# Optimization experiments

Hardware: AMD Instinct MI355X
Metric: run time of the kernel (lower is better)

The kernel has to match this reference:

```python
import jax, jax.numpy as jnp
import numpy as np

B, S, E, H, NE, K = 4, 1024, 1024, 16, 8, 2
DFF = 4 * E
DH = E // H
EPS = 1e-5


def _ln(x, g, b):
    m = jnp.mean(x, axis=-1, keepdims=True)
    v = jnp.mean(jnp.square(x - m), axis=-1, keepdims=True)
    return (x - m) * jax.lax.rsqrt(v + EPS) * g + b


def setup_inputs() -> dict:
    key = jax.random.key(0)
    ks = jax.random.split(key, 20)
    n = lambda k, sh, s: (jax.random.normal(k, sh, jnp.float32) * s)
    return {
        'x': n(ks[0], (B, S, E), 1.0),
        'ln1_g': jnp.ones((E,), jnp.float32), 'ln1_b': jnp.zeros((E,), jnp.float32),
        'wq': n(ks[1], (E, E), 0.02), 'bq': jnp.zeros((E,), jnp.float32),
        'wk': n(ks[2], (E, E), 0.02), 'bk': jnp.zeros((E,), jnp.float32),
        'wv': n(ks[3], (E, E), 0.02), 'bv': jnp.zeros((E,), jnp.float32),
        'wo': n(ks[4], (E, E), 0.02), 'bo': jnp.zeros((E,), jnp.float32),
        'ln2_g': jnp.ones((E,), jnp.float32), 'ln2_b': jnp.zeros((E,), jnp.float32),
        'sw1': n(ks[5], (E, DFF), 0.02), 'sb1': jnp.zeros((DFF,), jnp.float32),
        'sw2': n(ks[6], (DFF, E), 0.02), 'sb2': jnp.zeros((E,), jnp.float32),
        'ew1': n(ks[7], (NE, E, DFF), 0.02), 'eb1': jnp.zeros((NE, DFF), jnp.float32),
        'ew2': n(ks[8], (NE, DFF, E), 0.02), 'eb2': jnp.zeros((NE, E), jnp.float32),
        'w_gate': n(ks[9], (E, NE), 1.0),
    }


def reference(x, ln1_g, ln1_b, wq, bq, wk, bk, wv, bv, wo, bo,
              ln2_g, ln2_b, sw1, sb1, sw2, sb2, ew1, eb1, ew2, eb2, w_gate):
    # --- self-attention sublayer (eval: no dropout) ---
    res1 = x
    h = _ln(x, ln1_g, ln1_b)
    q = (h @ wq + bq).reshape(B, S, H, DH)
    k = (h @ wk + bk).reshape(B, S, H, DH)
    v = (h @ wv + bv).reshape(B, S, H, DH)
    scores = jnp.einsum('bqhd,bkhd->bhqk', q, k) / jnp.sqrt(jnp.float32(DH))
    attn = jax.nn.softmax(scores, axis=-1)
    ctx = jnp.einsum('bhqk,bkhd->bqhd', attn, v).reshape(B, S, E)
    x = res1 + (ctx @ wo + bo)

    # --- MoE sublayer ---
    res2 = x
    h2 = _ln(x, ln2_g, ln2_b)
    shared = jax.nn.gelu(h2 @ sw1 + sb1, approximate=False) @ sw2 + sb2

    # router (eval: clean logits, no noise)
    logits = h2 @ w_gate                                  # (B,S,NE)
    top_vals, top_idx = jax.lax.top_k(logits, K)          # (B,S,K)
    top_gates = jax.nn.softmax(top_vals, axis=-1)
    onehot = jax.nn.one_hot(top_idx, NE, dtype=x.dtype)   # (B,S,K,NE)
    gates = jnp.einsum('bsk,bske->bse', top_gates, onehot)
    probs = jax.nn.softmax(logits, axis=-1).reshape(-1, NE)
    P = probs.mean(0)
    f = (gates > 0).astype(x.dtype).reshape(-1, NE).mean(0)
    aux_loss = NE * jnp.sum(P * f)

    # dense all-expert compute, gated combine (matches original math)
    eh = jax.nn.gelu(jnp.einsum('bse,neh->bnsh', h2, ew1) + eb1[None, :, None, :],
                     approximate=False)
    eo = jnp.einsum('bnsh,nhe->bnse', eh, ew2) + eb2[None, :, None, :]
    expert_out = jnp.einsum('bnse,bsn->bse', eo, gates)

    return res2 + shared + expert_out, aux_loss
```

## Files before the change

### kernel.cpp

```cpp
#include <hip/hip_runtime.h>
#include <stdint.h>

#define B_    4
#define S_    1024
#define E_    1024
#define H_    16
#define NE_   8
#define DFF_  4096
#define NT_   4096
#define QS_   3072
#define ROWCAP9_ 13440

typedef unsigned short u16;
typedef short bf16x8 __attribute__((ext_vector_type(8)));
typedef float f32x4 __attribute__((ext_vector_type(4)));

__device__ __forceinline__ float bf2f(u16 u){ unsigned v = ((unsigned)u) << 16; return __builtin_bit_cast(float, v); }
__device__ __forceinline__ u16 f2bf(float f){ unsigned x = __builtin_bit_cast(unsigned, f); return (u16)((x + 0x7FFFu + ((x >> 16) & 1u)) >> 16); }
__device__ __forceinline__ float gelu_f(float x){ return 0.5f * x * (1.f + erff(x * 0.70710678118f)); }

__device__ __forceinline__ void gl_lds16(const u16* g, u16* l){
  __builtin_amdgcn_global_load_lds((__attribute__((address_space(1))) void*)(const_cast<u16*>(g)),
                                   (__attribute__((address_space(3))) void*)(l), 16, 0, 0);
}

#define KSW32(l)   ((((l) & 3) ^ (((l) >> 3) & 3)) << 3)
#define FRAGOFF(l) (((l) & 15) * 32 + (((((l) >> 4) ^ (((l) >> 1) & 3))) << 3))

__launch_bounds__(256)
__global__ void ln_kernel(const float* __restrict__ x, const float* __restrict__ g,
                          const float* __restrict__ be, u16* __restrict__ out)
{
  const int row = blockIdx.x;
  const float4 v = ((const float4*)(x + (size_t)row * E_))[threadIdx.x];
  float s = v.x + v.y + v.z + v.w;
  #pragma unroll
  for(int mm = 32; mm >= 1; mm >>= 1) s += __shfl_xor(s, mm);
  __shared__ float red[8];
  const int wid = threadIdx.x >> 6;
  if((threadIdx.x & 63) == 0) red[wid] = s;
  __syncthreads();
  const float mean = (red[0] + red[1] + red[2] + red[3]) * (1.0f / E_);
  const float d0 = v.x - mean, d1 = v.y - mean, d2 = v.z - mean, d3 = v.w - mean;
  float q2 = d0*d0 + d1*d1 + d2*d2 + d3*d3;
  #pragma unroll
  for(int mm = 32; mm >= 1; mm >>= 1) q2 += __shfl_xor(q2, mm);
  if((threadIdx.x & 63) == 0) red[4 + wid] = q2;
  __syncthreads();
  const float var = (red[4] + red[5] + red[6] + red[7]) * (1.0f / E_);
  const float rs = rsqrtf(var + 1e-5f);
  const float4 gg = ((const float4*)g)[threadIdx.x];
  const float4 bb = ((const float4*)be)[threadIdx.x];
  ushort4 o;
  o.x = f2bf(d0 * rs * gg.x + bb.x);
  o.y = f2bf(d1 * rs * gg.y + bb.y);
  o.z = f2bf(d2 * rs * gg.z + bb.z);
  o.w = f2bf(d3 * rs * gg.w + bb.w);
  ((ushort4*)(out + (size_t)row * E_))[threadIdx.x] = o;
}

__launch_bounds__(256)
__global__ void ln_router_kernel(const float* __restrict__ x, const float* __restrict__ g,
                                 const float* __restrict__ be, u16* __restrict__ out,
                                 const float* __restrict__ wg,
                                 float* __restrict__ probs, float* __restrict__ tkgate,
                                 int* __restrict__ tkidx, int* __restrict__ counts)
{
  const int row = blockIdx.x;
  const int tid = threadIdx.x, lane = tid & 63, wid = tid >> 6;
  const float4 v = ((const float4*)(x + (size_t)row * E_))[tid];
  float s = v.x + v.y + v.z + v.w;
  #pragma unroll
  for(int mm = 32; mm >= 1; mm >>= 1) s += __shfl_xor(s, mm);
  __shared__ float red[8];
  __shared__ float part[4][8];
  if(lane == 0) red[wid] = s;
  __syncthreads();
  const float mean = (red[0] + red[1] + red[2] + red[3]) * (1.0f / E_);
  const float d0 = v.x - mean, d1 = v.y - mean, d2 = v.z - mean, d3 = v.w - mean;
  float q2 = d0*d0 + d1*d1 + d2*d2 + d3*d3;
  #pragma unroll
  for(int mm = 32; mm >= 1; mm >>= 1) q2 += __shfl_xor(q2, mm);
  if(lane == 0) red[4 + wid] = q2;
  __syncthreads();
  const float var = (red[4] + red[5] + red[6] + red[7]) * (1.0f / E_);
  const float rs = rsqrtf(var + 1e-5f);
  const float4 gg = ((const float4*)g)[tid];
  const float4 bb = ((const float4*)be)[tid];
  ushort4 o;
  o.x = f2bf(d0 * rs * gg.x + bb.x);
  o.y = f2bf(d1 * rs * gg.y + bb.y);
  o.z = f2bf(d2 * rs * gg.z + bb.z);
  o.w = f2bf(d3 * rs * gg.w + bb.w);
  ((ushort4*)(out + (size_t)row * E_))[tid] = o;
  const float h0 = bf2f(o.x), h1 = bf2f(o.y), h2v = bf2f(o.z), h3 = bf2f(o.w);
  float a[8];
  #pragma unroll
  for(int e = 0; e < 8; e++) a[e] = 0.f;
  const float* wr = wg + (size_t)(tid * 4) * NE_;
  #pragma unroll
  for(int j = 0; j < 4; j++){
    const float hj = (j == 0) ? h0 : (j == 1) ? h1 : (j == 2) ? h2v : h3;
    const float4 w0 = *(const float4*)(wr + j * NE_);
    const float4 w1 = *(const float4*)(wr + j * NE_ + 4);
    a[0] += hj * w0.x; a[1] += hj * w0.y; a[2] += hj * w0.z; a[3] += hj * w0.w;
    a[4] += hj * w1.x; a[5] += hj * w1.y; a[6] += hj * w1.z; a[7] += hj * w1.w;
  }
  #pragma unroll
  for(int mm = 1; mm < 64; mm <<= 1)
    #pragma unroll
    for(int e = 0; e < 8; e++) a[e] += __shfl_xor(a[e], mm);
  if(lane == 0)
    #pragma unroll
    for(int e = 0; e < 8; e++) part[wid][e] = a[e];
  __syncthreads();
  if(tid == 0){
    float lg[8];
    #pragma unroll
    for(int e = 0; e < 8; e++) lg[e] = part[0][e] + part[1][e] + part[2][e] + part[3][e];
    float mx = lg[0];
    #pragma unroll
    for(int e = 1; e < 8; e++) mx = fmaxf(mx, lg[e]);
    float se = 0.f, ex[8];
    #pragma unroll
    for(int e = 0; e < 8; e++){ ex[e] = expf(lg[e] - mx); se += ex[e]; }
    const float inv = 1.f / se;
    float* pr = probs + (size_t)row * 8;
    #pragma unroll
    for(int e = 0; e < 8; e++) pr[e] = ex[e] * inv;
    int i1 = 0; float v1 = lg[0];
    #pragma unroll
    for(int e = 1; e < 8; e++) if(lg[e] > v1){ v1 = lg[e]; i1 = e; }
    int i2 = -1; float v2 = -3.4e38f;
    #pragma unroll
    for(int e = 0; e < 8; e++) if(e != i1 && lg[e] > v2){ v2 = lg[e]; i2 = e; }
    const float t = expf(v2 - v1);
    tkidx[row*2] = i1; tkidx[row*2+1] = i2;
    tkgate[row*2] = 1.f / (1.f + t); tkgate[row*2+1] = t / (1.f + t);
    atomicAdd(&counts[i1], 1); atomicAdd(&counts[i2], 1);
  }
}

__device__ __forceinline__ void transpose_body(const float* __restrict__ W, u16* __restrict__ WT, int K, int N)
{
  __shared__ __align__(16) u16 t[64][72];
  const int k0 = blockIdx.x * 64, n0 = blockIdx.y * 64;
  const int tid = threadIdx.x;
  const int kr = tid >> 2;
  const int nc = (tid & 3) * 4;
  #pragma unroll
  for(int p = 0; p < 4; p++){
    float4 v = *(const float4*)(W + (size_t)(k0 + kr) * N + n0 + nc + p * 16);
    t[nc + p*16 + 0][kr] = f2bf(v.x);
    t[nc + p*16 + 1][kr] = f2bf(v.y);
    t[nc + p*16 + 2][kr] = f2bf(v.z);
    t[nc + p*16 + 3][kr] = f2bf(v.w);
  }
  __syncthreads();
  const int nr = tid >> 3;
  const int kg = (tid & 7) * 8;
  #pragma unroll
  for(int p = 0; p < 2; p++){
    const int nn = nr + p * 32;
    unsigned u0 = t[nn][kg+0], u1 = t[nn][kg+1], u2 = t[nn][kg+2], u3 = t[nn][kg+3];
    unsigned u4 = t[nn][kg+4], u5 = t[nn][kg+5], u6 = t[nn][kg+6], u7 = t[nn][kg+7];
    uint4 o;
    o.x = u0 | (u1 << 16); o.y = u2 | (u3 << 16); o.z = u4 | (u5 << 16); o.w = u6 | (u7 << 16);
    *(uint4*)(WT + (size_t)(n0 + nn) * K + k0 + kg) = o;
  }
}

__launch_bounds__(256)
__global__ void transpose_kernel(const float* __restrict__ W, u16* __restrict__ WT, int K, int N)
{ transpose_body(W, WT, K, N); }

__launch_bounds__(256)
__global__ void transpose4_kernel(const float* wq, const float* wk, const float* wv, const float* wo,
                                  u16* __restrict__ WT)
{
  const float* W = (blockIdx.z == 0) ? wq : (blockIdx.z == 1) ? wk : (blockIdx.z == 2) ? wv : wo;
  transpose_body(W, WT + (size_t)blockIdx.z * E_ * E_, E_, E_);
}

__launch_bounds__(256)
__global__ void transpose9_kernel(const float* __restrict__ ew, const float* __restrict__ sw,
                                  u16* __restrict__ WT, int K, int N)
{
  const float* W = (blockIdx.z < 8) ? (ew + (size_t)blockIdx.z * K * N) : sw;
  transpose_body(W, WT + (size_t)blockIdx.z * K * N, K, N);
}

__global__ void prep_kernel(const float* __restrict__ bq, const float* __restrict__ bk,
                            const float* __restrict__ bv, float* __restrict__ bcat,
                            int* __restrict__ counts, int* __restrict__ rowlist,
                            const float* __restrict__ eb1, const float* __restrict__ sb1,
                            float* __restrict__ b9up,
                            const float* __restrict__ eb2, const float* __restrict__ sb2,
                            float* __restrict__ b9dn)
{
  const int stride = gridDim.x * 256;
  for(int i = blockIdx.x * 256 + threadIdx.x; i < 9 * DFF_; i += stride){
    b9up[i] = (i < 8 * DFF_) ? eb1[i] : sb1[i - 8 * DFF_];
    if(i < 9 * E_)   b9dn[i] = (i < 8 * E_) ? eb2[i] : sb2[i - 8 * E_];
    if(i < QS_)      bcat[i] = (i < E_) ? bq[i] : (i < 2*E_) ? bk[i - E_] : bv[i - 2*E_];
    if(i < 16)       counts[i] = 0;
    if(i < ROWCAP9_) rowlist[i] = -1;
  }
}

template<int MODE>
__launch_bounds__(256)
__global__ void gemm_kernel(const u16* __restrict__ A, const u16* __restrict__ Bt,
                            int N, int Kd, const float* __restrict__ bias,
                            u16* __restrict__ outB)
{
  __shared__ __align__(16) u16 As0[4096], Bs0[4096], As1[4096], Bs1[4096];
  const int tid = threadIdx.x, lane = tid & 63, wid = tid >> 6;
  const int wm = wid >> 1, wn = wid & 1;
  const int tm = blockIdx.y * 128, tn = blockIdx.x * 128;

  const f32x4 zero = {0.f, 0.f, 0.f, 0.f};
  f32x4 acc[4][4];
  #pragma unroll
  for(int m = 0; m < 4; m++)
    #pragma unroll
    for(int n = 0; n < 4; n++) acc[m][n] = zero;

  const int ksw = KSW32(lane);
  const u16* gA0 = A  + (size_t)(tm + wid*32 + (lane >> 2)) * Kd + ksw;
  const u16* gA1 = gA0 + (size_t)16 * Kd;
  const u16* gB0 = Bt + (size_t)(tn + wid*32 + (lane >> 2)) * Kd + ksw;
  const u16* gB1 = gB0 + (size_t)16 * Kd;
  u16* lA0 = As0 + wid*1024; u16* lA1 = lA0 + 512;
  u16* lB0 = Bs0 + wid*1024; u16* lB1 = lB0 + 512;
  u16* lA0b = As1 + wid*1024; u16* lA1b = lA0b + 512;
  u16* lB0b = Bs1 + wid*1024; u16* lB1b = lB0b + 512;
  const int fo = FRAGOFF(lane);
  const int fA = wm * 2048, fB = wn * 2048;

  for(int k0 = 0; k0 < Kd; k0 += 64){
    __syncthreads();
    gl_lds16(gA0 + k0, lA0);  gl_lds16(gA1 + k0, lA1);
    gl_lds16(gB0 + k0, lB0);  gl_lds16(gB1 + k0, lB1);
    gl_lds16(gA0 + k0+32, lA0b); gl_lds16(gA1 + k0+32, lA1b);
    gl_lds16(gB0 + k0+32, lB0b); gl_lds16(gB1 + k0+32, lB1b);
    __syncthreads();
    bf16x8 aF[4], bF[4];
    #pragma unroll
    for(int m = 0; m < 4; m++) aF[m] = *(const bf16x8*)(As0 + fA + m*512 + fo);
    #pragma unroll
    for(int n = 0; n < 4; n++) bF[n] = *(const bf16x8*)(Bs0 + fB + n*512 + fo);
    #pragma unroll
    for(int m = 0; m < 4; m++)
      #pragma unroll
      for(int n = 0; n < 4; n++)
        acc[m][n] = __builtin_amdgcn_mfma_f32_16x16x32_bf16(aF[m], bF[n], acc[m][n], 0, 0, 0);
    #pragma unroll
    for(int m = 0; m < 4; m++) aF[m] = *(const bf16x8*)(As1 + fA + m*512 + fo);
    #pragma unroll
    for(int n = 0; n < 4; n++) bF[n] = *(const bf16x8*)(Bs1 + fB + n*512 + fo);
    #pragma unroll
    for(int m = 0; m < 4; m++)
      #pragma unroll
      for(int n = 0; n < 4; n++)
        acc[m][n] = __builtin_amdgcn_mfma_f32_16x16x32_bf16(aF[m], bF[n], acc[m][n], 0, 0, 0);
  }

  #pragma unroll
  for(int m = 0; m < 4; m++){
    const int row = tm + wm*64 + m*16 + ((lane >> 4) << 2);
    #pragma unroll
    for(int n = 0; n < 4; n++){
      const int col = tn + wn*64 + n*16 + (lane & 15);
      const float bc = bias[col];
      #pragma unroll
      for(int r = 0; r < 4; r++){
        const float v = acc[m][n][r] + bc;
        const size_t idx = (size_t)(row + r) * N + col;
        if constexpr(MODE == 0) outB[idx] = f2bf(v);
        else outB[idx] = f2bf(gelu_f(v));
      }
    }
  }
}

template<int MODE>
__launch_bounds__(256)
__global__ void gemm64_kernel(const u16* __restrict__ A, const u16* __restrict__ Bt,
                              int N, int Kd, const float* __restrict__ bias,
                              float* __restrict__ outF, const float* __restrict__ resid)
{
  __shared__ __align__(16) u16 As0[2048], As1[2048], Bs0[4096], Bs1[4096];
  const int tid = threadIdx.x, lane = tid & 63, wid = tid >> 6;
  const int wm = wid >> 1, wn = wid & 1;
  const int tm = blockIdx.y * 64, tn = blockIdx.x * 128;

  const f32x4 zero = {0.f, 0.f, 0.f, 0.f};
  f32x4 acc[2][4];
  #pragma unroll
  for(int m = 0; m < 2; m++)
    #pragma unroll
    for(int n = 0; n < 4; n++) acc[m][n] = zero;

  const int ksw = KSW32(lane);
  const u16* gA = A + (size_t)(tm + wid*16 + (lane >> 2)) * Kd + ksw;
  const u16* gB0 = Bt + (size_t)(tn + wid*32 + (lane >> 2)) * Kd + ksw;
  const u16* gB1 = gB0 + (size_t)16 * Kd;
  u16* lA  = As0 + wid*512;  u16* lAb = As1 + wid*512;
  u16* lB0 = Bs0 + wid*1024; u16* lB1 = lB0 + 512;
  u16* lB0b = Bs1 + wid*1024; u16* lB1b = lB0b + 512;
  const int fo = FRAGOFF(lane);
  const int fA = wm * 1024, fB = wn * 2048;

  for(int k0 = 0; k0 < Kd; k0 += 64){
    __syncthreads();
    gl_lds16(gA + k0, lA);
    gl_lds16(gB0 + k0, lB0); gl_lds16(gB1 + k0, lB1);
    gl_lds16(gA + k0+32, lAb);
    gl_lds16(gB0 + k0+32, lB0b); gl_lds16(gB1 + k0+32, lB1b);
    __syncthreads();
    bf16x8 aF[2], bF[4];
    #pragma unroll
    for(int m = 0; m < 2; m++) aF[m] = *(const bf16x8*)(As0 + fA + m*512 + fo);
    #pragma unroll
    for(int n = 0; n < 4; n++) bF[n] = *(const bf16x8*)(Bs0 + fB + n*512 + fo);
    #pragma unroll
    for(int m = 0; m < 2; m++)
      #pragma unroll
      for(int n = 0; n < 4; n++)
        acc[m][n] = __builtin_amdgcn_mfma_f32_16x16x32_bf16(aF[m], bF[n], acc[m][n], 0, 0, 0);
    #pragma unroll
    for(int m = 0; m < 2; m++) aF[m] = *(const bf16x8*)(As1 + fA + m*512 + fo);
    #pragma unroll
    for(int n = 0; n < 4; n++) bF[n] = *(const bf16x8*)(Bs1 + fB + n*512 + fo);
    #pragma unroll
    for(int m = 0; m < 2; m++)
      #pragma unroll
      for(int n = 0; n < 4; n++)
        acc[m][n] = __builtin_amdgcn_mfma_f32_16x16x32_bf16(aF[m], bF[n], acc[m][n], 0, 0, 0);
  }

  #pragma unroll
  for(int m = 0; m < 2; m++){
    const int row = tm + wm*32 + m*16 + ((lane >> 4) << 2);
    #pragma unroll
    for(int n = 0; n < 4; n++){
      const int col = tn + wn*64 + n*16 + (lane & 15);
      const float bc = bias[col];
      #pragma unroll
      for(int r = 0; r < 4; r++){
        const float v = acc[m][n][r] + bc;
        const size_t idx = (size_t)(row + r) * N + col;
        if constexpr(MODE == 2) outF[idx] = resid[idx] + v;
        else outF[idx] += v;
      }
    }
  }
}

__launch_bounds__(256)
__global__ void attn_kernel(const u16* __restrict__ qkv, u16* __restrict__ ctx)
{
  __shared__ __align__(16) u16 Ks[64 * 64];
  __shared__ __align__(16) u16 Vt[64 * 72];
  __shared__ __align__(16) u16 Ps[64 * 72];
  const int tid = threadIdx.x, lane = tid & 63, wid = tid >> 6;
  const int bh = blockIdx.y, bb = bh >> 4, hh = bh & 15;
  const int q0 = blockIdx.x * 64;
  const size_t tok0 = (size_t)bb * S_;
  const int hcol = hh * 64;

  bf16x8 aQ0, aQ1;
  {
    const u16* qp = qkv + (tok0 + q0 + wid*16 + (lane & 15)) * QS_ + hcol + ((lane >> 4) << 3);
    aQ0 = *(const bf16x8*)qp;
    aQ1 = *(const bf16x8*)(qp + 32);
  }
  const f32x4 zero = {0.f, 0.f, 0.f, 0.f};
  f32x4 accO[4]; float mrow[4], lrow[4];
  #pragma unroll
  for(int n = 0; n < 4; n++) accO[n] = zero;
  #pragma unroll
  for(int r = 0; r < 4; r++){ mrow[r] = -1e30f; lrow[r] = 0.f; }
  const float sc = 0.125f * 1.44269504f;
  const int ksw8 = (((lane & 7) ^ ((lane >> 3) & 7)) << 3);

  for(int kv0 = 0; kv0 < S_; kv0 += 64){
    __syncthreads();
    {
      const u16* gp = qkv + (tok0 + kv0 + wid*16 + (lane >> 3)) * QS_ + 1024 + hcol + ksw8;
      gl_lds16(gp, Ks + (wid*16) * 64);
      gl_lds16(gp + (size_t)8 * QS_, Ks + (wid*16 + 8) * 64);
    }
    {
      #pragma unroll
      for(int i = 0; i < 2; i++){
        const int tok = (tid >> 3) + i * 32;
        const int d0 = (tid & 7) << 3;
        bf16x8 vv = *(const bf16x8*)(qkv + (tok0 + kv0 + tok) * QS_ + 2048 + hcol + d0);
        #pragma unroll
        for(int j = 0; j < 8; j++) Vt[(d0 + j) * 72 + tok] = (u16)vv[j];
      }
    }
    __syncthreads();
    f32x4 sf[4];
    #pragma unroll
    for(int n = 0; n < 4; n++){
      const int rb = n*16 + (lane & 15);
      bf16x8 b0 = *(const bf16x8*)(Ks + rb*64 + ((((lane >> 4)    ) ^ (lane & 7)) << 3));
      bf16x8 b1 = *(const bf16x8*)(Ks + rb*64 + ((((lane >> 4) + 4) ^ (lane & 7)) << 3));
      f32x4 t = zero;
      t = __builtin_amdgcn_mfma_f32_16x16x32_bf16(aQ0, b0, t, 0, 0, 0);
      t = __builtin_amdgcn_mfma_f32_16x16x32_bf16(aQ1, b1, t, 0, 0, 0);
      sf[n] = t;
    }
    #pragma unroll
    for(int r = 0; r < 4; r++){
      const float s0 = sf[0][r]*sc, s1 = sf[1][r]*sc, s2 = sf[2][r]*sc, s3 = sf[3][r]*sc;
      float mx = fmaxf(fmaxf(s0, s1), fmaxf(s2, s3));
      #pragma unroll
      for(int mm = 1; mm < 16; mm <<= 1) mx = fmaxf(mx, __shfl_xor(mx, mm));
      const float mnew = fmaxf(mrow[r], mx);
      const float resc = exp2f(mrow[r] - mnew);
      mrow[r] = mnew;
      const float p0 = exp2f(s0 - mnew), p1 = exp2f(s1 - mnew);
      const float p2 = exp2f(s2 - mnew), p3 = exp2f(s3 - mnew);
      float ps = p0 + p1 + p2 + p3;
      #pragma unroll
      for(int mm = 1; mm < 16; mm <<= 1) ps += __shfl_xor(ps, mm);
      lrow[r] = lrow[r] * resc + ps;
      #pragma unroll
      for(int n = 0; n < 4; n++) accO[n][r] *= resc;
      const int prow = wid*16 + ((lane >> 4) << 2) + r;
      Ps[prow*72 +      (lane & 15)] = f2bf(p0);
      Ps[prow*72 + 16 + (lane & 15)] = f2bf(p1);
      Ps[prow*72 + 32 + (lane & 15)] = f2bf(p2);
      Ps[prow*72 + 48 + (lane & 15)] = f2bf(p3);
    }
    bf16x8 pa0 = *(const bf16x8*)(Ps + (wid*16 + (lane & 15)) * 72 + ((lane >> 4) << 3));
    bf16x8 pa1 = *(const bf16x8*)(Ps + (wid*16 + (lane & 15)) * 72 + 32 + ((lane >> 4) << 3));
    #pragma unroll
    for(int n = 0; n < 4; n++){
      bf16x8 b0 = *(const bf16x8*)(Vt + (n*16 + (lane & 15)) * 72 + ((lane >> 4) << 3));
      bf16x8 b1 = *(const bf16x8*)(Vt + (n*16 + (lane & 15)) * 72 + 32 + ((lane >> 4) << 3));
      accO[n] = __builtin_amdgcn_mfma_f32_16x16x32_bf16(pa0, b0, accO[n], 0, 0, 0);
      accO[n] = __builtin_amdgcn_mfma_f32_16x16x32_bf16(pa1, b1, accO[n], 0, 0, 0);
    }
  }
  const size_t cbase = tok0 * E_ + hcol;
  #pragma unroll
  for(int n = 0; n < 4; n++)
    #pragma unroll
    for(int r = 0; r < 4; r++){
      const int row = q0 + wid*16 + ((lane >> 4) << 2) + r;
      const int col = n*16 + (lane & 15);
      ctx[cbase + (size_t)row * E_ + col] = f2bf(accO[n][r] / lrow[r]);
    }
}

__global__ void scan_kernel(const int* __restrict__ counts, int* __restrict__ aoff,
                            int* __restrict__ cursor, int addShared)
{
  if(threadIdx.x == 0){
    int o = 0;
    for(int e = 0; e < 8; e++){
      aoff[e] = o; cursor[e] = o;
      o += ((counts[e] + 127) >> 7) << 7;
    }
    aoff[8] = o;
    aoff[9] = o + (addShared ? NT_ : 0);
  }
}

__global__ void build_kernel(const int* __restrict__ tkidx, const float* __restrict__ tkgate,
                             int* __restrict__ cursor, int* __restrict__ rowlist,
                             float* __restrict__ rowgate, const int* __restrict__ aoff, int addShared)
{
  const int t = blockIdx.x * 256 + threadIdx.x;
  if(t >= NT_) return;
  #pragma unroll
  for(int kk = 0; kk < 2; kk++){
    const int e = tkidx[t*2 + kk];
    const int pos = atomicAdd(&cursor[e], 1);
    rowlist[pos] = t; rowgate[pos] = tkgate[t*2 + kk];
  }
  if(addShared){
    const int base = aoff[8];
    rowlist[base + t] = t; rowgate[base + t] = 1.f;
  }
}

__launch_bounds__(256)
__global__ void upmoe_kernel(const u16* __restrict__ Ah2, const u16* __restrict__ W1T,
                             const float* __restrict__ b9up,
                             const int* __restrict__ rowlist, const int* __restrict__ aoff,
                             u16* __restrict__ ehid)
{
  const int rowTile = blockIdx.y * 128;
  if(rowTile >= aoff[9]) return;
  int e = 0;
  #pragma unroll
  for(int i = 1; i <= 8; i++) if(rowTile >= aoff[i]) e = i;
  __shared__ __align__(16) u16 As0[4096], Bs0[4096], As1[4096], Bs1[4096];
  const int tid = threadIdx.x, lane = tid & 63, wid = tid >> 6;
  const int wm = wid >> 1, wn = wid & 1;
  const int tn = blockIdx.x * 128;
  const u16* Bt = W1T + (size_t)e * DFF_ * E_;

  const int r0 = rowTile + wid*32 + (lane >> 2);
  int t0 = rowlist[r0];      if(t0 < 0) t0 = 0;
  int t1 = rowlist[r0 + 16]; if(t1 < 0) t1 = 0;
  const int ksw = KSW32(lane);
  const u16* gA0 = Ah2 + (size_t)t0 * E_ + ksw;
  const u16* gA1 = Ah2 + (size_t)t1 * E_ + ksw;
  const u16* gB0 = Bt + (size_t)(tn + wid*32 + (lane >> 2)) * E_ + ksw;
  const u16* gB1 = gB0 + (size_t)16 * E_;
  u16* lA0 = As0 + wid*1024; u16* lA1 = lA0 + 512;
  u16* lB0 = Bs0 + wid*1024; u16* lB1 = lB0 + 512;
  u16* lA0b = As1 + wid*1024; u16* lA1b = lA0b + 512;
  u16* lB0b = Bs1 + wid*1024; u16* lB1b = lB0b + 512;
  const int fo = FRAGOFF(lane);
  const int fA = wm * 2048, fB = wn * 2048;

  const f32x4 zero = {0.f,0.f,0.f,0.f};
  f32x4 acc[4][4];
  #pragma unroll
  for(int m = 0; m < 4; m++)
    #pragma unroll
    for(int n = 0; n < 4; n++) acc[m][n] = zero;

  for(int k0 = 0; k0 < E_; k0 += 64){
    __syncthreads();
    gl_lds16(gA0 + k0, lA0);  gl_lds16(gA1 + k0, lA1);
    gl_lds16(gB0 + k0, lB0);  gl_lds16(gB1 + k0, lB1);
    gl_lds16(gA0 + k0+32, lA0b); gl_lds16(gA1 + k0+32, lA1b);
    gl_lds16(gB0 + k0+32, lB0b); gl_lds16(gB1 + k0+32, lB1b);
    __syncthreads();
    bf16x8 aF[4], bF[4];
    #pragma unroll
    for(int m = 0; m < 4; m++) aF[m] = *(const bf16x8*)(As0 + fA + m*512 + fo);
    #pragma unroll
    for(int n = 0; n < 4; n++) bF[n] = *(const bf16x8*)(Bs0 + fB + n*512 + fo);
    #pragma unroll
    for(int m = 0; m < 4; m++)
      #pragma unroll
      for(int n = 0; n < 4; n++)
        acc[m][n] = __builtin_amdgcn_mfma_f32_16x16x32_bf16(aF[m], bF[n], acc[m][n], 0, 0, 0);
    #pragma unroll
    for(int m = 0; m < 4; m++) aF[m] = *(const bf16x8*)(As1 + fA + m*512 + fo);
    #pragma unroll
    for(int n = 0; n < 4; n++) bF[n] = *(const bf16x8*)(Bs1 + fB + n*512 + fo);
    #pragma unroll
    for(int m = 0; m < 4; m++)
      #pragma unroll
      for(int n = 0; n < 4; n++)
        acc[m][n] = __builtin_amdgcn_mfma_f32_16x16x32_bf16(aF[m], bF[n], acc[m][n], 0, 0, 0);
  }
  #pragma unroll
  for(int m = 0; m < 4; m++){
    const int row = rowTile + wm*64 + m*16 + ((lane >> 4) << 2);
    #pragma unroll
    for(int n = 0; n < 4; n++){
      const int col = tn + wn*64 + n*16 + (lane & 15);
      const float bc = b9up[e * DFF_ + col];
      #pragma unroll
      for(int r = 0; r < 4; r++)
        ehid[(size_t)(row + r) * DFF_ + col] = f2bf(gelu_f(acc[m][n][r] + bc));
    }
  }
}

__launch_bounds__(256)
__global__ void downmoe_kernel(const u16* __restrict__ ehid, const u16* __restrict__ W2T,
                               const float* __restrict__ b9dn,
                               const int* __restrict__ rowlist, const float* __restrict__ rowgate,
                               const int* __restrict__ aoff, float* __restrict__ outF)
{
  const int nwg = (int)(gridDim.x * gridDim.y);
  const int b_lin = (int)(blockIdx.x + blockIdx.y * gridDim.x);
  const int b2 = (b_lin & 7) * (nwg >> 3) + (b_lin >> 3);
  const int bx = b2 & 7, by = b2 >> 3;
  const int rowTile = by * 64;
  if(rowTile >= aoff[9]) return;
  int e = 0;
  #pragma unroll
  for(int i = 1; i <= 8; i++) if(rowTile >= aoff[i]) e = i;
  __shared__ __align__(16) u16 As0[2048], As1[2048], Bs0[4096], Bs1[4096];
  const int tid = threadIdx.x, lane = tid & 63, wid = tid >> 6;
  const int wm = wid >> 1, wn = wid & 1;
  const int tn = bx * 128;
  const u16* Bt = W2T + (size_t)e * E_ * DFF_;

  const int ksw = KSW32(lane);
  const u16* gA = ehid + (size_t)(rowTile + wid*16 + (lane >> 2)) * DFF_ + ksw;
  const u16* gB0 = Bt + (size_t)(tn + wid*32 + (lane >> 2)) * DFF_ + ksw;
  const u16* gB1 = gB0 + (size_t)16 * DFF_;
  u16* lA  = As0 + wid*512;  u16* lAb = As1 + wid*512;
  u16* lB0 = Bs0 + wid*1024; u16* lB1 = lB0 + 512;
  u16* lB0b = Bs1 + wid*1024; u16* lB1b = lB0b + 512;
  const int fo = FRAGOFF(lane);
  const int fA = wm * 1024, fB = wn * 2048;

  const f32x4 zero = {0.f,0.f,0.f,0.f};
  f32x4 acc[2][4];
  #pragma unroll
  for(int m = 0; m < 2; m++)
    #pragma unroll
    for(int n = 0; n < 4; n++) acc[m][n] = zero;

  for(int k0 = 0; k0 < DFF_; k0 += 64){
    __syncthreads();
    gl_lds16(gA + k0, lA);
    gl_lds16(gB0 + k0, lB0); gl_lds16(gB1 + k0, lB1);
    gl_lds16(gA + k0+32, lAb);
    gl_lds16(gB0 + k0+32, lB0b); gl_lds16(gB1 + k0+32, lB1b);
    __syncthreads();
    bf16x8 aF[2], bF[4];
    #pragma unroll
    for(int m = 0; m < 2; m++) aF[m] = *(const bf16x8*)(As0 + fA + m*512 + fo);
    #pragma unroll
    for(int n = 0; n < 4; n++) bF[n] = *(const bf16x8*)(Bs0 + fB + n*512 + fo);
    #pragma unroll
    for(int m = 0; m < 2; m++)
      #pragma unroll
      for(int n = 0; n < 4; n++)
        acc[m][n] = __builtin_amdgcn_mfma_f32_16x16x32_bf16(aF[m], bF[n], acc[m][n], 0, 0, 0);
    #pragma unroll
    for(int m = 0; m < 2; m++) aF[m] = *(const bf16x8*)(As1 + fA + m*512 + fo);
    #pragma unroll
    for(int n = 0; n < 4; n++) bF[n] = *(const bf16x8*)(Bs1 + fB + n*512 + fo);
    #pragma unroll
    for(int m = 0; m < 2; m++)
      #pragma unroll
      for(int n = 0; n < 4; n++)
        acc[m][n] = __builtin_amdgcn_mfma_f32_16x16x32_bf16(aF[m], bF[n], acc[m][n], 0, 0, 0);
  }
  #pragma unroll
  for(int m = 0; m < 2; m++){
    const int row = rowTile + wm*32 + m*16 + ((lane >> 4) << 2);
    #pragma unroll
    for(int r = 0; r < 4; r++){
      const int rr = row + r;
      const int tok = rowlist[rr];
      if(tok < 0) continue;
      const float g = rowgate[rr];
      #pragma unroll
      for(int n = 0; n < 4; n++){
        const int col = tn + wn*64 + n*16 + (lane & 15);
        atomicAdd(&outF[(size_t)tok * E_ + col], g * (acc[m][n][r] + b9dn[e * E_ + col]));
      }
    }
  }
}

__launch_bounds__(256)
__global__ void aux_kernel(const float* __restrict__ probs, const int* __restrict__ counts,
                           float* __restrict__ outaux)
{
  float a[8];
  #pragma unroll
  for(int e = 0; e < 8; e++) a[e] = 0.f;
  for(int t = threadIdx.x; t < NT_; t += 256){
    const float* p = probs + (size_t)t * 8;
    #pragma unroll
    for(int e = 0; e < 8; e++) a[e] += p[e];
  }
  #pragma unroll
  for(int mm = 1; mm < 64; mm <<= 1)
    #pragma unroll
    for(int e = 0; e < 8; e++) a[e] += __shfl_xor(a[e], mm);
  __shared__ float part[4][8];
  const int wid = threadIdx.x >> 6;
  if((threadIdx.x & 63) == 0)
    for(int e = 0; e < 8; e++) part[wid][e] = a[e];
  __syncthreads();
  if(threadIdx.x == 0){
    float aux = 0.f;
    for(int e = 0; e < 8; e++){
      const float P = (part[0][e] + part[1][e] + part[2][e] + part[3][e]) / (float)NT_;
      const float f = (float)counts[e] / (float)NT_;
      aux += P * f;
    }
    outaux[0] = (float)NE_ * aux;
  }
}

extern "C" void kernel_launch(void* const* d_in, const int* in_sizes, int n_in,
                              void* d_out, int out_size, void* d_ws, size_t ws_size,
                              hipStream_t stream)
{
  (void)in_sizes; (void)n_in; (void)out_size;
  const float* x    = (const float*)d_in[0];
  const float* ln1g = (const float*)d_in[1];
  const float* ln1b = (const float*)d_in[2];
  const float* wq   = (const float*)d_in[3];
  const float* bq   = (const float*)d_in[4];
  const float* wk   = (const float*)d_in[5];
  const float* bk   = (const float*)d_in[6];
  const float* wv   = (const float*)d_in[7];
  const float* bv   = (const float*)d_in[8];
  const float* wo   = (const float*)d_in[9];
  const float* bo   = (const float*)d_in[10];
  const float* ln2g = (const float*)d_in[11];
  const float* ln2b = (const float*)d_in[12];
  const float* sw1  = (const float*)d_in[13];
  const float* sb1  = (const float*)d_in[14];
  const float* sw2  = (const float*)d_in[15];
  const float* sb2  = (const float*)d_in[16];
  const float* ew1  = (const float*)d_in[17];
  const float* eb1  = (const float*)d_in[18];
  const float* ew2  = (const float*)d_in[19];
  const float* eb2  = (const float*)d_in[20];
  const float* wgate= (const float*)d_in[21];
  float* out = (float*)d_out;
  char* ws = (char*)d_ws;
  const size_t MB = 1024ull * 1024ull;
  const bool big = (ws_size >= 194 * MB);

  char* rt = big ? (ws + 192*MB) : (ws + 24*MB);
  float* probs   = (float*)(rt);
  float* tkgate  = (float*)(rt + 131072);
  int*   tkidx   = (int*)  (rt + 163840);
  int*   counts  = (int*)  (rt + 196608);
  int*   aoff    = (int*)  (rt + 196672);
  int*   cursor  = (int*)  (rt + 196736);
  int*   rowlist = (int*)  (rt + 196800);
  float* rowgate = (float*)(rt + 250560);
  float* bcat    = (float*)(rt + 304320);
  float* b9up    = (float*)(rt + 316608);
  float* b9dn    = (float*)(rt + 464064);

  if(big){
    u16* h    = (u16*)(ws + 0);
    u16* qkvb = (u16*)(ws + 8*MB);
    u16* ctx  = (u16*)(ws + 32*MB);
    u16* wT4  = (u16*)(ws + 40*MB);
    u16* ehid = (u16*)(ws + 0);
    u16* W1T  = (u16*)(ws + 112*MB);
    u16* W2T  = W1T;
    u16* h2   = (u16*)(ws + 184*MB);

    prep_kernel<<<64, 256, 0, stream>>>(bq, bk, bv, bcat, counts, rowlist, eb1, sb1, b9up, eb2, sb2, b9dn);
    transpose4_kernel<<<dim3(16,16,4), 256, 0, stream>>>(wq, wk, wv, wo, wT4);
    transpose9_kernel<<<dim3(16,64,9), 256, 0, stream>>>(ew1, sw1, W1T, E_, DFF_);
    ln_kernel<<<NT_, 256, 0, stream>>>(x, ln1g, ln1b, h);
    gemm_kernel<0><<<dim3(24,32), 256, 0, stream>>>(h, wT4, QS_, E_, bcat, qkvb);
    attn_kernel<<<dim3(16,64), 256, 0, stream>>>(qkvb, ctx);
    gemm64_kernel<2><<<dim3(8,64), 256, 0, stream>>>(ctx, wT4 + 3u*1024*1024, E_, E_, bo, out, x);
    ln_router_kernel<<<NT_, 256, 0, stream>>>(out, ln2g, ln2b, h2, wgate, probs, tkgate, tkidx, counts);
    scan_kernel<<<1, 64, 0, stream>>>(counts, aoff, cursor, 1);
    build_kernel<<<16, 256, 0, stream>>>(tkidx, tkgate, cursor, rowlist, rowgate, aoff, 1);
    upmoe_kernel<<<dim3(32,104), 256, 0, stream>>>(h2, W1T, b9up, rowlist, aoff, ehid);
    transpose9_kernel<<<dim3(64,16,9), 256, 0, stream>>>(ew2, sw2, W2T, DFF_, E_);
    downmoe_kernel<<<dim3(8,208), 256, 0, stream>>>(ehid, W2T, b9dn, rowlist, rowgate, aoff, out);
    aux_kernel<<<1, 256, 0, stream>>>(probs, counts, out + (size_t)NT_ * E_);
  } else {
    u16* h    = (u16*)(ws + 0);
    u16* h2   = (u16*)(ws + 8*MB);
    u16* wT4  = (u16*)(ws + 16*MB);
    u16* swT  = wT4;
    u16* qkvb = (u16*)(ws + 32*MB);
    u16* ctx  = (u16*)(ws + 56*MB);
    u16* hidS = (u16*)(ws + 64*MB);
    u16* ewT  = (u16*)(ws + 32*MB);
    u16* ehid = (u16*)(ws + 96*MB);

    prep_kernel<<<64, 256, 0, stream>>>(bq, bk, bv, bcat, counts, rowlist, eb1, sb1, b9up, eb2, sb2, b9dn);
    transpose4_kernel<<<dim3(16,16,4), 256, 0, stream>>>(wq, wk, wv, wo, wT4);
    ln_kernel<<<NT_, 256, 0, stream>>>(x, ln1g, ln1b, h);
    gemm_kernel<0><<<dim3(24,32), 256, 0, stream>>>(h, wT4, QS_, E_, bcat, qkvb);
    attn_kernel<<<dim3(16,64), 256, 0, stream>>>(qkvb, ctx);
    gemm64_kernel<2><<<dim3(8,64), 256, 0, stream>>>(ctx, wT4 + 3u*1024*1024, E_, E_, bo, out, x);
    ln_router_kernel<<<NT_, 256, 0, stream>>>(out, ln2g, ln2b, h2, wgate, probs, tkgate, tkidx, counts);
    transpose_kernel<<<dim3(16,64), 256, 0, stream>>>(sw1, swT, E_, DFF_);
    gemm_kernel<1><<<dim3(32,32), 256, 0, stream>>>(h2, swT, DFF_, E_, sb1, hidS);
    transpose_kernel<<<dim3(64,16), 256, 0, stream>>>(sw2, swT, DFF_, E_);
    gemm64_kernel<3><<<dim3(8,64), 256, 0, stream>>>(hidS, swT, E_, DFF_, sb2, out, nullptr);
    scan_kernel<<<1, 64, 0, stream>>>(counts, aoff, cursor, 0);
    build_kernel<<<16, 256, 0, stream>>>(tkidx, tkgate, cursor, rowlist, rowgate, aoff, 0);
    transpose9_kernel<<<dim3(16,64,8), 256, 0, stream>>>(ew1, sw1, ewT, E_, DFF_);
    upmoe_kernel<<<dim3(32,104), 256, 0, stream>>>(h2, ewT, b9up, rowlist, aoff, ehid);
    transpose9_kernel<<<dim3(64,16,8), 256, 0, stream>>>(ew2, sw2, ewT, DFF_, E_);
    downmoe_kernel<<<dim3(8,208), 256, 0, stream>>>(ehid, ewT, b9dn, rowlist, rowgate, aoff, out);
    aux_kernel<<<1, 256, 0, stream>>>(probs, counts, out + (size_t)NT_ * E_);
  }
}
```

Before: 791.4 us.

## Double-buffer downmoe K-loop and fuse scan/build/aux into one route kernel

The down-projection MoE GEMM now prefetches the next 64-wide K slice into a second LDS buffer while computing on the current one. It uses vmcnt waits and raw barriers instead of two syncthreads per iteration, which doubles LDS use per block and may lower occupancy. Separately, the scan, build and aux-loss kernels are merged into one single-block route kernel to cut two launches. The merged kernel does the row-list build in one block with LDS atomics, trading parallelism for fewer launches.

After: 806.9 us. About the same (+2.0%).

```diff
diff --git a/kernel.cpp b/kernel.cpp
--- a/kernel.cpp
+++ b/kernel.cpp
@@ -26,6 +26,8 @@
 
 #define KSW32(l)   ((((l) & 3) ^ (((l) >> 3) & 3)) << 3)
 #define FRAGOFF(l) (((l) & 15) * 32 + (((((l) >> 4) ^ (((l) >> 1) & 3))) << 3))
+
+#define VMCNT(n)   asm volatile("s_waitcnt vmcnt(" #n ")" ::: "memory")
 
 __launch_bounds__(256)
 __global__ void ln_kernel(const float* __restrict__ x, const float* __restrict__ g,
@@ -208,6 +210,59 @@
   }
 }
 
+__launch_bounds__(256)
+__global__ void route_kernel(const int* __restrict__ counts, const int* __restrict__ tkidx,
+                             const float* __restrict__ tkgate, const float* __restrict__ probs,
+                             int* __restrict__ aoff, int* __restrict__ rowlist,
+                             float* __restrict__ rowgate, float* __restrict__ outaux, int addShared)
+{
+  __shared__ int cur[8];
+  __shared__ int aoffs[10];
+  __shared__ float part[4][8];
+  const int tid = threadIdx.x, lane = tid & 63, wid = tid >> 6;
+  if(tid == 0){
+    int o = 0;
+    for(int e = 0; e < 8; e++){ aoffs[e] = o; cur[e] = o; o += ((counts[e] + 127) >> 7) << 7; }
+    aoffs[8] = o; aoffs[9] = o + (addShared ? NT_ : 0);
+    for(int e = 0; e < 10; e++) aoff[e] = aoffs[e];
+  }
+  __syncthreads();
+  for(int t = tid; t < NT_; t += 256){
+    #pragma unroll
+    for(int kk = 0; kk < 2; kk++){
+      const int e = tkidx[t*2 + kk];
+      const int pos = atomicAdd(&cur[e], 1);
+      rowlist[pos] = t; rowgate[pos] = tkgate[t*2 + kk];
+    }
+    if(addShared){ rowlist[aoffs[8] + t] = t; rowgate[aoffs[8] + t] = 1.f; }
+  }
+  float a[8];
+  #pragma unroll
+  for(int e = 0; e < 8; e++) a[e] = 0.f;
+  for(int t = tid; t < NT_; t += 256){
+    const float* p = probs + (size_t)t * 8;
+    #pragma unroll
+    for(int e = 0; e < 8; e++) a[e] += p[e];
+  }
+  #pragma unroll
+  for(int mm = 1; mm < 64; mm <<= 1)
+    #pragma unroll
+    for(int e = 0; e < 8; e++) a[e] += __shfl_xor(a[e], mm);
+  if(lane == 0)
+    #pragma unroll
+    for(int e = 0; e < 8; e++) part[wid][e] = a[e];
+  __syncthreads();
+  if(tid == 0){
+    float aux = 0.f;
+    for(int e = 0; e < 8; e++){
+      const float P = (part[0][e] + part[1][e] + part[2][e] + part[3][e]) / (float)NT_;
+      const float f = (float)counts[e] / (float)NT_;
+      aux += P * f;
+    }
+    outaux[0] = (float)NE_ * aux;
+  }
+}
+
 template<int MODE>
 __launch_bounds__(256)
 __global__ void gemm_kernel(const u16* __restrict__ A, const u16* __restrict__ Bt,
@@ -456,38 +511,6 @@
       const int col = n*16 + (lane & 15);
       ctx[cbase + (size_t)row * E_ + col] = f2bf(accO[n][r] / lrow[r]);
     }
-}
-
-__global__ void scan_kernel(const int* __restrict__ counts, int* __restrict__ aoff,
-                            int* __restrict__ cursor, int addShared)
-{
-  if(threadIdx.x == 0){
-    int o = 0;
-    for(int e = 0; e < 8; e++){
-      aoff[e] = o; cursor[e] = o;
-      o += ((counts[e] + 127) >> 7) << 7;
-    }
-    aoff[8] = o;
-    aoff[9] = o + (addShared ? NT_ : 0);
-  }
-}
-
-__global__ void build_kernel(const int* __restrict__ tkidx, const float* __restrict__ tkgate,
-                             int* __restrict__ cursor, int* __restrict__ rowlist,
-                             float* __restrict__ rowgate, const int* __restrict__ aoff, int addShared)
-{
-  const int t = blockIdx.x * 256 + threadIdx.x;
-  if(t >= NT_) return;
-  #pragma unroll
-  for(int kk = 0; kk < 2; kk++){
-    const int e = tkidx[t*2 + kk];
-    const int pos = atomicAdd(&cursor[e], 1);
-    rowlist[pos] = t; rowgate[pos] = tkgate[t*2 + kk];
-  }
-  if(addShared){
-    const int base = aoff[8];
-    rowlist[base + t] = t; rowgate[base + t] = 1.f;
-  }
 }
 
 __launch_bounds__(256)
@@ -585,7 +608,7 @@
   int e = 0;
   #pragma unroll
   for(int i = 1; i <= 8; i++) if(rowTile >= aoff[i]) e = i;
-  __shared__ __align__(16) u16 As0[2048], As1[2048], Bs0[4096], Bs1[4096];
+  __shared__ __align__(16) u16 As[2][4096], Bs[2][8192];
   const int tid = threadIdx.x, lane = tid & 63, wid = tid >> 6;
   const int wm = wid >> 1, wn = wid & 1;
   const int tn = bx * 128;
@@ -595,9 +618,7 @@
   const u16* gA = ehid + (size_t)(rowTile + wid*16 + (lane >> 2)) * DFF_ + ksw;
   const u16* gB0 = Bt + (size_t)(tn + wid*32 + (lane >> 2)) * DFF_ + ksw;
   const u16* gB1 = gB0 + (size_t)16 * DFF_;
-  u16* lA  = As0 + wid*512;  u16* lAb = As1 + wid*512;
-  u16* lB0 = Bs0 + wid*1024; u16* lB1 = lB0 + 512;
-  u16* lB0b = Bs1 + wid*1024; u16* lB1b = lB0b + 512;
+  const int segA = wid * 512, segB = wid * 1024;
   const int fo = FRAGOFF(lane);
   const int fA = wm * 1024, fB = wn * 2048;
 
@@ -608,33 +629,44 @@
     #pragma unroll
     for(int n = 0; n < 4; n++) acc[m][n] = zero;
 
-  for(int k0 = 0; k0 < DFF_; k0 += 64){
-    __syncthreads();
-    gl_lds16(gA + k0, lA);
-    gl_lds16(gB0 + k0, lB0); gl_lds16(gB1 + k0, lB1);
-    gl_lds16(gA + k0+32, lAb);
-    gl_lds16(gB0 + k0+32, lB0b); gl_lds16(gB1 + k0+32, lB1b);
-    __syncthreads();
+  auto stage = [&](int t, int cb){
+    const int ko = t << 6;
+    gl_lds16(gA + ko, &As[cb][segA]);
+    gl_lds16(gB0 + ko, &Bs[cb][segB]); gl_lds16(gB1 + ko, &Bs[cb][segB + 512]);
+    gl_lds16(gA + ko + 32, &As[cb][2048 + segA]);
+    gl_lds16(gB0 + ko + 32, &Bs[cb][4096 + segB]); gl_lds16(gB1 + ko + 32, &Bs[cb][4096 + segB + 512]);
+  };
+  auto compute = [&](int cb){
     bf16x8 aF[2], bF[4];
     #pragma unroll
-    for(int m = 0; m < 2; m++) aF[m] = *(const bf16x8*)(As0 + fA + m*512 + fo);
-    #pragma unroll
-    for(int n = 0; n < 4; n++) bF[n] = *(const bf16x8*)(Bs0 + fB + n*512 + fo);
-    #pragma unroll
-    for(int m = 0; m < 2; m++)
-      #pragma unroll
-      for(int n = 0; n < 4; n++)
-        acc[m][n] = __builtin_amdgcn_mfma_f32_16x16x32_bf16(aF[m], bF[n], acc[m][n], 0, 0, 0);
-    #pragma unroll
-    for(int m = 0; m < 2; m++) aF[m] = *(const bf16x8*)(As1 + fA + m*512 + fo);
-    #pragma unroll
-    for(int n = 0; n < 4; n++) bF[n] = *(const bf16x8*)(Bs1 + fB + n*512 + fo);
-    #pragma unroll
-    for(int m = 0; m < 2; m++)
-      #pragma unroll
-      for(int n = 0; n < 4; n++)
-        acc[m][n] = __builtin_amdgcn_mfma_f32_16x16x32_bf16(aF[m], bF[n], acc[m][n], 0, 0, 0);
-  }
+    for(int h = 0; h < 2; h++){
+      const u16* as = &As[cb][h * 2048];
+      const u16* bs = &Bs[cb][h * 4096];
+      #pragma unroll
+      for(int m = 0; m < 2; m++) aF[m] = *(const bf16x8*)(as + fA + m*512 + fo);
+      #pragma unroll
+      for(int n = 0; n < 4; n++) bF[n] = *(const bf16x8*)(bs + fB + n*512 + fo);
+      #pragma unroll
+      for(int m = 0; m < 2; m++)
+        #pragma unroll
+        for(int n = 0; n < 4; n++)
+          acc[m][n] = __builtin_amdgcn_mfma_f32_16x16x32_bf16(aF[m], bF[n], acc[m][n], 0, 0, 0);
+    }
+  };
+
+  const int nt = DFF_ >> 6;
+  stage(0, 0);
+  for(int t = 0; t < nt - 1; ++t){
+    stage(t + 1, (t + 1) & 1);
+    VMCNT(6);
+    __builtin_amdgcn_s_barrier();
+    compute(t & 1);
+    __builtin_amdgcn_s_barrier();
+  }
+  VMCNT(0);
+  __builtin_amdgcn_s_barrier();
+  compute((nt - 1) & 1);
+
   #pragma unroll
   for(int m = 0; m < 2; m++){
     const int row = rowTile + wm*32 + m*16 + ((lane >> 4) << 2);
@@ -650,38 +682,6 @@
         atomicAdd(&outF[(size_t)tok * E_ + col], g * (acc[m][n][r] + b9dn[e * E_ + col]));
       }
     }
-  }
-}
-
-__launch_bounds__(256)
-__global__ void aux_kernel(const float* __restrict__ probs, const int* __restrict__ counts,
-                           float* __restrict__ outaux)
-{
-  float a[8];
-  #pragma unroll
-  for(int e = 0; e < 8; e++) a[e] = 0.f;
-  for(int t = threadIdx.x; t < NT_; t += 256){
-    const float* p = probs + (size_t)t * 8;
-    #pragma unroll
-    for(int e = 0; e < 8; e++) a[e] += p[e];
-  }
-  #pragma unroll
-  for(int mm = 1; mm < 64; mm <<= 1)
-    #pragma unroll
-    for(int e = 0; e < 8; e++) a[e] += __shfl_xor(a[e], mm);
-  __shared__ float part[4][8];
-  const int wid = threadIdx.x >> 6;
-  if((threadIdx.x & 63) == 0)
-    for(int e = 0; e < 8; e++) part[wid][e] = a[e];
-  __syncthreads();
-  if(threadIdx.x == 0){
-    float aux = 0.f;
-    for(int e = 0; e < 8; e++){
-      const float P = (part[0][e] + part[1][e] + part[2][e] + part[3][e]) / (float)NT_;
-      const float f = (float)counts[e] / (float)NT_;
-      aux += P * f;
-    }
-    outaux[0] = (float)NE_ * aux;
   }
 }
 
@@ -723,7 +723,6 @@
   int*   tkidx   = (int*)  (rt + 163840);
   int*   counts  = (int*)  (rt + 196608);
   int*   aoff    = (int*)  (rt + 196672);
-  int*   cursor  = (int*)  (rt + 196736);
   int*   rowlist = (int*)  (rt + 196800);
   float* rowgate = (float*)(rt + 250560);
   float* bcat    = (float*)(rt + 304320);
@@ -748,12 +747,11 @@
     attn_kernel<<<dim3(16,64), 256, 0, stream>>>(qkvb, ctx);
     gemm64_kernel<2><<<dim3(8,64), 256, 0, stream>>>(ctx, wT4 + 3u*1024*1024, E_, E_, bo, out, x);
     ln_router_kernel<<<NT_, 256, 0, stream>>>(out, ln2g, ln2b, h2, wgate, probs, tkgate, tkidx, counts);
-    scan_kernel<<<1, 64, 0, stream>>>(counts, aoff, cursor, 1);
-    build_kernel<<<16, 256, 0, stream>>>(tkidx, tkgate, cursor, rowlist, rowgate, aoff, 1);
+    route_kernel<<<1, 256, 0, stream>>>(counts, tkidx, tkgate, probs, aoff, rowlist, rowgate,
+                                        out + (size_t)NT_ * E_, 1);
     upmoe_kernel<<<dim3(32,104), 256, 0, stream>>>(h2, W1T, b9up, rowlist, aoff, ehid);
     transpose9_kernel<<<dim3(64,16,9), 256, 0, stream>>>(ew2, sw2, W2T, DFF_, E_);
     downmoe_kernel<<<dim3(8,208), 256, 0, stream>>>(ehid, W2T, b9dn, rowlist, rowgate, aoff, out);
-    aux_kernel<<<1, 256, 0, stream>>>(probs, counts, out + (size_t)NT_ * E_);
   } else {
     u16* h    = (u16*)(ws + 0);
     u16* h2   = (u16*)(ws + 8*MB);
@@ -776,12 +774,11 @@
     gemm_kernel<1><<<dim3(32,32), 256, 0, stream>>>(h2, swT, DFF_, E_, sb1, hidS);
     transpose_kernel<<<dim3(64,16), 256, 0, stream>>>(sw2, swT, DFF_, E_);
     gemm64_kernel<3><<<dim3(8,64), 256, 0, stream>>>(hidS, swT, E_, DFF_, sb2, out, nullptr);
-    scan_kernel<<<1, 64, 0, stream>>>(counts, aoff, cursor, 0);
-    build_kernel<<<16, 256, 0, stream>>>(tkidx, tkgate, cursor, rowlist, rowgate, aoff, 0);
+    route_kernel<<<1, 256, 0, stream>>>(counts, tkidx, tkgate, probs, aoff, rowlist, rowgate,
+                                        out + (size_t)NT_ * E_, 0);
     transpose9_kernel<<<dim3(16,64,8), 256, 0, stream>>>(ew1, sw1, ewT, E_, DFF_);
     upmoe_kernel<<<dim3(32,104), 256, 0, stream>>>(h2, ewT, b9up, rowlist, aoff, ehid);
     transpose9_kernel<<<dim3(64,16,8), 256, 0, stream>>>(ew2, sw2, ewT, DFF_, E_);
     downmoe_kernel<<<dim3(8,208), 256, 0, stream>>>(ehid, ewT, b9dn, rowlist, rowgate, aoff, out);
-    aux_kernel<<<1, 256, 0, stream>>>(probs, counts, out + (size_t)NT_ * E_);
-  }
-}
+  }
+}
```
